# Optimization experiments

Measured on AMD Instinct MI355X. Metric: run time of the kernel, lower is better.

## Reference

```python
import jax, jax.numpy as jnp
import numpy as np

B, T = 64, 512
VOCAB, E, H = 20, 64, 128
D = 2 * H            # 256, bidirectional LSTM output dim
NH, KD = 8, D // 8   # 8 heads, key_dim 32
DU, OUT = 256, 128
NEG = -1e9


def _lstm_scan(x, mask, W, U, b):
    # x: [B,T,E], mask: [B,T] bool. Keras gate order: i, f, g(c), o.
    Bb = x.shape[0]
    Hh = U.shape[0]
    def step(carry, inp):
        h, c = carry
        xt, mt = inp                      # [B,E], [B]
        z = xt @ W + h @ U + b            # [B,4H]
        i, f, g, o = jnp.split(z, 4, axis=-1)
        c_new = jax.nn.sigmoid(f) * c + jax.nn.sigmoid(i) * jnp.tanh(g)
        h_new = jax.nn.sigmoid(o) * jnp.tanh(c_new)
        m = mt[:, None]
        h = jnp.where(m, h_new, h)        # freeze state/output on masked steps
        c = jnp.where(m, c_new, c)
        return (h, c), h
    h0 = jnp.zeros((Bb, Hh), x.dtype)
    _, ys = jax.lax.scan(step, (h0, h0), (jnp.swapaxes(x, 0, 1), mask.T))
    return jnp.swapaxes(ys, 0, 1)         # [B,T,H]


def setup_inputs() -> dict:
    key = jax.random.key(0)
    ks = jax.random.split(key, 24)
    g = lambda k, shape, s: (jax.random.normal(k, shape, jnp.float32) * s)
    inp = {
        'sequences': jax.random.randint(ks[0], (B, T), 0, VOCAB),
        'emb': g(ks[1], (VOCAB, E), 0.05),
        # forward LSTM
        'Wf': g(ks[2], (E, 4 * H), 0.05), 'Uf': g(ks[3], (H, 4 * H), 0.05), 'bf': jnp.zeros((4 * H,), jnp.float32),
        # backward LSTM
        'Wb': g(ks[4], (E, 4 * H), 0.05), 'Ub': g(ks[5], (H, 4 * H), 0.05), 'bb': jnp.zeros((4 * H,), jnp.float32),
        # MHA projections
        'Wq': g(ks[6], (D, NH, KD), 0.05), 'bq': jnp.zeros((NH, KD), jnp.float32),
        'Wk': g(ks[7], (D, NH, KD), 0.05), 'bk': jnp.zeros((NH, KD), jnp.float32),
        'Wv': g(ks[8], (D, NH, KD), 0.05), 'bv': jnp.zeros((NH, KD), jnp.float32),
        'Wo': g(ks[9], (NH, KD, D), 0.05), 'bo': jnp.zeros((D,), jnp.float32),
        # MLP head (input is concat of avg+max pool -> 2*D)
        'W1': g(ks[10], (2 * D, DU), 0.05), 'b1': jnp.zeros((DU,), jnp.float32),
        'W2': g(ks[11], (DU, DU // 2), 0.05), 'b2': jnp.zeros((DU // 2,), jnp.float32),
        'W3': g(ks[12], (DU // 2, OUT), 0.05), 'b3': jnp.zeros((OUT,), jnp.float32),
    }
    return inp


def _forward(sequences, emb, Wf, Uf, bf, Wb, Ub, bb, Wq, bq, Wk, bk, Wv, bv, Wo, bo, W1, b1, W2, b2, W3, b3):
    mask = sequences != 0                       # mask_zero=True
    x = emb[sequences]                          # [B,T,E]
    fwd = _lstm_scan(x, mask, Wf, Uf, bf)
    bwd = _lstm_scan(x[:, ::-1], mask[:, ::-1], Wb, Ub, bb)[:, ::-1]
    h = jnp.concatenate([fwd, bwd], axis=-1)    # [B,T,D]
    # Multi-head self-attention (key-masked, Keras MHA math)
    q = jnp.einsum('btd,dhk->bthk', h, Wq) + bq
    k = jnp.einsum('btd,dhk->bthk', h, Wk) + bk
    v = jnp.einsum('btd,dhk->bthk', h, Wv) + bv
    scores = jnp.einsum('bthk,bshk->bhts', q, k) / jnp.sqrt(jnp.float32(KD))
    scores = jnp.where(mask[:, None, None, :], scores, NEG)
    attn = jax.nn.softmax(scores, axis=-1)      # [B,H,T,T]
    ctx = jnp.einsum('bhts,bshk->bthk', attn, v)
    att = jnp.einsum('bthk,hkd->btd', ctx, Wo) + bo   # [B,T,D]
    # dual pooling (masked mean + masked max)
    mf = mask[..., None].astype(att.dtype)
    avg = (att * mf).sum(axis=1) / jnp.maximum(mf.sum(axis=1), 1.0)
    mx = jnp.where(mask[..., None], att, NEG).max(axis=1)
    p = jnp.concatenate([avg, mx], axis=-1)     # [B,2D]
    x1 = jax.nn.relu(p @ W1 + b1)
    x2 = jax.nn.relu(x1 @ W2 + b2)
    return x2 @ W3 + b3                         # [B,OUT]


def reference(sequences, emb, Wf, Uf, bf, Wb, Ub, bb, Wq, bq, Wk, bk, Wv, bv, Wo, bo, W1, b1, W2, b2, W3, b3):
    return _forward(sequences, emb, Wf, Uf, bf, Wb, Ub, bb, Wq, bq, Wk, bk, Wv, bv, Wo, bo, W1, b1, W2, b2, W3, b3)
```

## Files before the change

### kernel.cpp

```cpp
#include <hip/hip_runtime.h>
#include <math.h>

#define B_ 64
#define T_ 512
#define E_ 64
#define H_ 128
#define NH_ 8
#define KD_ 32
#define BT_ (B_ * T_)
#define NEG_ -1e9f

typedef __attribute__((ext_vector_type(8))) short bf16x8_t;
typedef __attribute__((ext_vector_type(4))) float f32x4_t;
typedef unsigned short ushort_t;
typedef unsigned int uint_t;

__device__ __forceinline__ float sigmoidf_(float x) {
    return 1.f / (1.f + __expf(-x));
}
__device__ __forceinline__ float tanhf_(float x) {
    return 1.f - 2.f / (1.f + __expf(2.f * x));
}

__device__ __forceinline__ ushort_t bf16_rne(float x) {
    uint_t u = __float_as_uint(x);
    uint_t r = (u + 0x7FFFu + ((u >> 16) & 1u)) >> 16;
    return (ushort_t)r;
}
__device__ __forceinline__ float bf16_to_f(ushort_t h) {
    return __uint_as_float(((uint_t)h) << 16);
}
__device__ __forceinline__ void split_bf16(float x, ushort_t& h, ushort_t& l) {
    h = bf16_rne(x);
    l = bf16_rne(x - bf16_to_f(h));
}

__device__ __forceinline__ float qswap1(float x) {
    return __int_as_float(__builtin_amdgcn_mov_dpp(__float_as_int(x), 0xB1, 0xF, 0xF, true));
}
__device__ __forceinline__ float qswap2(float x) {
    return __int_as_float(__builtin_amdgcn_mov_dpp(__float_as_int(x), 0x4E, 0xF, 0xF, true));
}

template <bool GATHER, bool PERM>
__global__ __launch_bounds__(256, 3) void gemm_f32(
    const float* __restrict__ A, const int* __restrict__ gidx,
    const float* __restrict__ emb, const float* __restrict__ Bm,
    const float* __restrict__ bias, float* __restrict__ C,
    int M, int N, int K)
{
    __shared__ __align__(16) float As[16][132];
    __shared__ __align__(16) float Bs[16][128];
    const int tid = threadIdx.x;
    const int tx = tid & 15, ty = tid >> 4;
    const int ntn = N >> 7;
    const int bm = blockIdx.x / ntn, bn = blockIdx.x % ntn;
    const int m0 = bm << 7, n0 = bn << 7;

    float acc[8][8];
#pragma unroll
    for (int i = 0; i < 8; ++i)
#pragma unroll
        for (int j = 0; j < 8; ++j) acc[i][j] = 0.f;

    const int ac4 = (tid & 3) << 2;
    const int ar  = tid >> 2;
    const int bc4 = (tid & 31) << 2;
    const int br  = tid >> 5;

    for (int k0 = 0; k0 < K; k0 += 16) {
        __syncthreads();
#pragma unroll
        for (int p = 0; p < 2; ++p) {
            const int r = ar + p * 64;
            const int gm = m0 + r;
            const float* src = GATHER
                ? (emb + (size_t)gidx[gm] * K + (k0 + ac4))
                : (A + (size_t)gm * K + (k0 + ac4));
            float4 v = *(const float4*)src;
            As[ac4 + 0][r] = v.x; As[ac4 + 1][r] = v.y;
            As[ac4 + 2][r] = v.z; As[ac4 + 3][r] = v.w;
        }
#pragma unroll
        for (int p = 0; p < 2; ++p) {
            const int rr = br + p * 8;
            if (PERM) {
                const float* brow = Bm + (size_t)(k0 + rr) * N;
                const int base = (n0 >> 2) + (tid & 31);
                Bs[rr][bc4 + 0] = brow[base];
                Bs[rr][bc4 + 1] = brow[128 + base];
                Bs[rr][bc4 + 2] = brow[256 + base];
                Bs[rr][bc4 + 3] = brow[384 + base];
            } else {
                float4 v = *(const float4*)(Bm + (size_t)(k0 + rr) * N + (n0 + bc4));
                *(float4*)&Bs[rr][bc4] = v;
            }
        }
        __syncthreads();
#pragma unroll
        for (int k = 0; k < 16; ++k) {
            float a[8], b[8];
            *(float4*)&a[0] = *(const float4*)&As[k][ty << 3];
            *(float4*)&a[4] = *(const float4*)&As[k][(ty << 3) + 4];
            *(float4*)&b[0] = *(const float4*)&Bs[k][tx << 3];
            *(float4*)&b[4] = *(const float4*)&Bs[k][(tx << 3) + 4];
#pragma unroll
            for (int i = 0; i < 8; ++i)
#pragma unroll
                for (int j = 0; j < 8; ++j)
                    acc[i][j] = fmaf(a[i], b[j], acc[i][j]);
        }
    }

    float bv[8];
#pragma unroll
    for (int j = 0; j < 8; ++j) {
        const int n = n0 + (tx << 3) + j;
        bv[j] = PERM ? bias[((n & 3) << 7) + (n >> 2)] : bias[n];
    }
#pragma unroll
    for (int i = 0; i < 8; ++i) {
        float* dst = C + (size_t)(m0 + (ty << 3) + i) * N + n0 + (tx << 3);
        float4 o0 = { acc[i][0] + bv[0], acc[i][1] + bv[1],
                      acc[i][2] + bv[2], acc[i][3] + bv[3] };
        float4 o1 = { acc[i][4] + bv[4], acc[i][5] + bv[5],
                      acc[i][6] + bv[6], acc[i][7] + bv[7] };
        *(float4*)dst = o0;
        *(float4*)(dst + 4) = o1;
    }
}

__global__ void wconv(const float* __restrict__ W,
                      ushort_t* __restrict__ Bh, ushort_t* __restrict__ Bl)
{
    const int k = blockIdx.x, n = threadIdx.x;
    float v = W[k * 256 + n];
    ushort_t h, l;
    split_bf16(v, h, l);
    Bh[n * 256 + k] = h;
    Bl[n * 256 + k] = l;
}

__global__ __launch_bounds__(256, 2) void gemm_mfma3(
    const ushort_t* __restrict__ Ah, const ushort_t* __restrict__ Al,
    const ushort_t* __restrict__ Bh, const ushort_t* __restrict__ Bl,
    const float* __restrict__ bias, float* __restrict__ C,
    int M, int N)
{
    __shared__ __align__(16) ushort_t Alds[2][128 * 40];
    __shared__ __align__(16) ushort_t Blds[2][128 * 40];

    const int tid = threadIdx.x;
    const int ntn = N >> 7;
    const int bm = blockIdx.x / ntn, bn = blockIdx.x % ntn;
    const int m0 = bm << 7, n0 = bn << 7;

    const int w = tid >> 6;
    const int wr = w >> 1, wc = w & 1;
    const int lane = tid & 63;
    const int fr = lane & 15, kg = lane >> 4;

    const int sr = tid >> 1;
    const int sh = (tid & 1) << 4;

    f32x4_t acc[4][4];
#pragma unroll
    for (int i = 0; i < 4; ++i)
#pragma unroll
        for (int j = 0; j < 4; ++j) acc[i][j] = (f32x4_t){0.f, 0.f, 0.f, 0.f};

    for (int ks = 0; ks < 8; ++ks) {
        const int k0 = ks << 5;
        __syncthreads();
        {
            const size_t ga = (size_t)(m0 + sr) * 256 + k0 + sh;
            const size_t gb = (size_t)(n0 + sr) * 256 + k0 + sh;
            const int ld = sr * 40 + sh;
            const uint4* pah = (const uint4*)(Ah + ga);
            const uint4* pal = (const uint4*)(Al + ga);
            const uint4* pbh = (const uint4*)(Bh + gb);
            const uint4* pbl = (const uint4*)(Bl + gb);
            uint4* qah = (uint4*)&Alds[0][ld];
            uint4* qal = (uint4*)&Alds[1][ld];
            uint4* qbh = (uint4*)&Blds[0][ld];
            uint4* qbl = (uint4*)&Blds[1][ld];
            qah[0] = pah[0]; qah[1] = pah[1];
            qal[0] = pal[0]; qal[1] = pal[1];
            qbh[0] = pbh[0]; qbh[1] = pbh[1];
            qbl[0] = pbl[0]; qbl[1] = pbl[1];
        }
        __syncthreads();

        bf16x8_t ah[4], al[4], bh[4], bl[4];
#pragma unroll
        for (int i = 0; i < 4; ++i) {
            const int ra = (wr * 64 + i * 16 + fr) * 40 + kg * 8;
            const int rb = (wc * 64 + i * 16 + fr) * 40 + kg * 8;
            ah[i] = *(const bf16x8_t*)&Alds[0][ra];
            al[i] = *(const bf16x8_t*)&Alds[1][ra];
            bh[i] = *(const bf16x8_t*)&Blds[0][rb];
            bl[i] = *(const bf16x8_t*)&Blds[1][rb];
        }
#pragma unroll
        for (int i = 0; i < 4; ++i)
#pragma unroll
            for (int j = 0; j < 4; ++j) {
                acc[i][j] = __builtin_amdgcn_mfma_f32_16x16x32_bf16(
                    ah[i], bh[j], acc[i][j], 0, 0, 0);
                acc[i][j] = __builtin_amdgcn_mfma_f32_16x16x32_bf16(
                    ah[i], bl[j], acc[i][j], 0, 0, 0);
                acc[i][j] = __builtin_amdgcn_mfma_f32_16x16x32_bf16(
                    al[i], bh[j], acc[i][j], 0, 0, 0);
            }
    }

#pragma unroll
    for (int j = 0; j < 4; ++j) {
        const int col = n0 + wc * 64 + j * 16 + fr;
        const float bv = bias[col];
#pragma unroll
        for (int i = 0; i < 4; ++i) {
#pragma unroll
            for (int r = 0; r < 4; ++r) {
                const int row = m0 + wr * 64 + i * 16 + kg * 4 + r;
                C[(size_t)row * N + col] = acc[i][j][r] + bv;
            }
        }
    }
}

__global__ __launch_bounds__(512, 1) void lstm_scan(
    const int* __restrict__ seq,
    const float* __restrict__ xwf, const float* __restrict__ xwb,
    const float* __restrict__ Uf, const float* __restrict__ Ub,
    ushort_t* __restrict__ hch, ushort_t* __restrict__ hcl)
{
    const int w = blockIdx.x;
    const int dir = w & 1, b = w >> 1;
    const float* xw = dir ? xwb : xwf;
    const float* U  = dir ? Ub  : Uf;
    const int tid = threadIdx.x;
    const int jj = tid >> 2, ks = tid & 3;

    __shared__ __align__(16) float hbuf[2][4][36];
    __shared__ float mkl[T_];

    float u[4][32];
#pragma unroll
    for (int g = 0; g < 4; ++g)
#pragma unroll
        for (int kk = 0; kk < 32; ++kk)
            u[g][kk] = U[(size_t)(32 * ks + kk) * 512 + g * 128 + jj];

    mkl[tid] = (seq[b * T_ + tid] != 0) ? 1.f : 0.f;
    if (tid < 2 * 4 * 36) ((float*)hbuf)[tid] = 0.f;

    float h_cur = 0.f, c_cur = 0.f;
    ushort_t* hoh = hch + (size_t)b * T_ * 256 + dir * 128;
    ushort_t* hol = hcl + (size_t)b * T_ * 256 + dir * 128;
    const float* xr = xw + (size_t)b * T_ * 512;

    __syncthreads();

    int te = dir ? (T_ - 1) : 0;
    float4 xwv = *(const float4*)&xr[(size_t)te * 512 + jj * 4];

    int p = 0;
    for (int t = 0; t < T_; ++t) {
        const int te_n  = dir ? (te - 1) : (te + 1);
        const int te_pf = (t == T_ - 1) ? te : te_n;
        const float4 xw_n = *(const float4*)&xr[(size_t)te_pf * 512 + jj * 4];

        float a0 = 0.f, a1 = 0.f, a2 = 0.f, a3 = 0.f;
        const float* hc = hbuf[p][ks];
#pragma unroll
        for (int c = 0; c < 8; ++c) {
            const float4 h4 = *(const float4*)&hc[c * 4];
            a0 = fmaf(h4.x, u[0][c*4+0], a0); a0 = fmaf(h4.y, u[0][c*4+1], a0);
            a0 = fmaf(h4.z, u[0][c*4+2], a0); a0 = fmaf(h4.w, u[0][c*4+3], a0);
            a1 = fmaf(h4.x, u[1][c*4+0], a1); a1 = fmaf(h4.y, u[1][c*4+1], a1);
            a1 = fmaf(h4.z, u[1][c*4+2], a1); a1 = fmaf(h4.w, u[1][c*4+3], a1);
            a2 = fmaf(h4.x, u[2][c*4+0], a2); a2 = fmaf(h4.y, u[2][c*4+1], a2);
            a2 = fmaf(h4.z, u[2][c*4+2], a2); a2 = fmaf(h4.w, u[2][c*4+3], a2);
            a3 = fmaf(h4.x, u[3][c*4+0], a3); a3 = fmaf(h4.y, u[3][c*4+1], a3);
            a3 = fmaf(h4.z, u[3][c*4+2], a3); a3 = fmaf(h4.w, u[3][c*4+3], a3);
        }
        a0 += qswap1(a0); a0 += qswap2(a0);
        a1 += qswap1(a1); a1 += qswap2(a1);
        a2 += qswap1(a2); a2 += qswap2(a2);
        a3 += qswap1(a3); a3 += qswap2(a3);

        const float zi = xwv.x + a0, zf = xwv.y + a1;
        const float zg = xwv.z + a2, zo = xwv.w + a3;
        const float cn = fmaf(sigmoidf_(zf), c_cur, sigmoidf_(zi) * tanhf_(zg));
        const float hn = sigmoidf_(zo) * tanhf_(cn);
        const float m  = mkl[te];
        const float hm = (m > 0.5f) ? hn : h_cur;
        c_cur = (m > 0.5f) ? cn : c_cur;
        h_cur = hm;

        if ((jj >> 5) == ks) hbuf[1 - p][ks][jj & 31] = hm;
        if (ks == 0) {
            ushort_t hh, hl;
            split_bf16(hm, hh, hl);
            hoh[(size_t)te * 256 + jj] = hh;
            hol[(size_t)te * 256 + jj] = hl;
        }
        __syncthreads();
        p ^= 1; te = te_n; xwv = xw_n;
    }
}

__global__ __launch_bounds__(256, 2) void attn_fused(
    const int* __restrict__ seq,
    const float* __restrict__ q, const float* __restrict__ kk,
    const float* __restrict__ vv,
    ushort_t* __restrict__ cxh, ushort_t* __restrict__ cxl)
{
    const int wg = blockIdx.x;
    const int b = wg >> 3, h = wg & 7;
    const int tid = threadIdx.x;

    __shared__ __align__(16) float Ks[16][32];
    __shared__ __align__(16) float Vs[16][32];
    __shared__ float mk[16];

    float qA[32], qB[32];
    {
        const float* qp  = q + (((size_t)(b * T_) + tid) * NH_ + h) * KD_;
        const float* qp2 = qp + (size_t)256 * NH_ * KD_;
#pragma unroll
        for (int k = 0; k < 32; k += 4) {
            float4 v0 = *(const float4*)(qp + k);
            float4 v1 = *(const float4*)(qp2 + k);
            qA[k] = v0.x; qA[k + 1] = v0.y; qA[k + 2] = v0.z; qA[k + 3] = v0.w;
            qB[k] = v1.x; qB[k + 1] = v1.y; qB[k + 2] = v1.z; qB[k + 3] = v1.w;
        }
    }
    float ctxA[32], ctxB[32];
#pragma unroll
    for (int k = 0; k < 32; ++k) { ctxA[k] = 0.f; ctxB[k] = 0.f; }
    float mA = -1e30f, mB = -1e30f, lA = 0.f, lB = 0.f;

    const int lr = (tid & 127) >> 3;
    const int lc = (tid & 7) << 2;
    const bool loadV = (tid >= 128);

    for (int c = 0; c < T_ / 16; ++c) {
        const int s0 = c << 4;
        __syncthreads();
        {
            const float* src = (loadV ? vv : kk) +
                (((size_t)(b * T_) + s0 + lr) * NH_ + h) * KD_ + lc;
            float4 v = *(const float4*)src;
            if (loadV) *(float4*)&Vs[lr][lc] = v;
            else       *(float4*)&Ks[lr][lc] = v;
            if (tid < 16) mk[tid] = (seq[b * T_ + s0 + tid] != 0) ? 0.f : 1.f;
        }
        __syncthreads();

        float sA[16], sB[16];
#pragma unroll
        for (int s = 0; s < 16; ++s) {
            float dA = 0.f, dB = 0.f;
#pragma unroll
            for (int k = 0; k < 32; k += 4) {
                float4 k4 = *(const float4*)&Ks[s][k];
                dA = fmaf(k4.x, qA[k], dA); dA = fmaf(k4.y, qA[k + 1], dA);
                dA = fmaf(k4.z, qA[k + 2], dA); dA = fmaf(k4.w, qA[k + 3], dA);
                dB = fmaf(k4.x, qB[k], dB); dB = fmaf(k4.y, qB[k + 1], dB);
                dB = fmaf(k4.z, qB[k + 2], dB); dB = fmaf(k4.w, qB[k + 3], dB);
            }
            const float SCL = 0.17677669529663687f;
            const bool masked = (mk[s] > 0.5f);
            sA[s] = masked ? NEG_ : dA * SCL;
            sB[s] = masked ? NEG_ : dB * SCL;
        }
        float cmA = sA[0], cmB = sB[0];
#pragma unroll
        for (int s = 1; s < 16; ++s) {
            cmA = fmaxf(cmA, sA[s]); cmB = fmaxf(cmB, sB[s]);
        }
        const float mnA = fmaxf(mA, cmA), mnB = fmaxf(mB, cmB);
        const float alA = __expf(mA - mnA), alB = __expf(mB - mnB);
        float psA = 0.f, psB = 0.f;
#pragma unroll
        for (int s = 0; s < 16; ++s) {
            float pa = __expf(sA[s] - mnA); sA[s] = pa; psA += pa;
            float pb = __expf(sB[s] - mnB); sB[s] = pb; psB += pb;
        }
        lA = fmaf(lA, alA, psA); lB = fmaf(lB, alB, psB);
        mA = mnA; mB = mnB;
#pragma unroll
        for (int k = 0; k < 32; ++k) { ctxA[k] *= alA; ctxB[k] *= alB; }
#pragma unroll
        for (int s = 0; s < 16; ++s) {
#pragma unroll
            for (int k = 0; k < 32; k += 4) {
                float4 v4 = *(const float4*)&Vs[s][k];
                ctxA[k]     = fmaf(sA[s], v4.x, ctxA[k]);
                ctxA[k + 1] = fmaf(sA[s], v4.y, ctxA[k + 1]);
                ctxA[k + 2] = fmaf(sA[s], v4.z, ctxA[k + 2]);
                ctxA[k + 3] = fmaf(sA[s], v4.w, ctxA[k + 3]);
                ctxB[k]     = fmaf(sB[s], v4.x, ctxB[k]);
                ctxB[k + 1] = fmaf(sB[s], v4.y, ctxB[k + 1]);
                ctxB[k + 2] = fmaf(sB[s], v4.z, ctxB[k + 2]);
                ctxB[k + 3] = fmaf(sB[s], v4.w, ctxB[k + 3]);
            }
        }
    }

    const float iA = 1.f / lA, iB = 1.f / lB;
    ushort_t* chA = cxh + (((size_t)(b * T_) + tid) * NH_ + h) * KD_;
    ushort_t* clA = cxl + (((size_t)(b * T_) + tid) * NH_ + h) * KD_;
    ushort_t* chB = chA + (size_t)256 * NH_ * KD_;
    ushort_t* clB = clA + (size_t)256 * NH_ * KD_;
#pragma unroll
    for (int k = 0; k < 32; ++k) {
        ushort_t hA, lA_, hB, lB_;
        split_bf16(ctxA[k] * iA, hA, lA_);
        split_bf16(ctxB[k] * iB, hB, lB_);
        chA[k] = hA; clA[k] = lA_;
        chB[k] = hB; clB[k] = lB_;
    }
}

__global__ void pool_kernel(const int* __restrict__ seq,
                            const float* __restrict__ att,
                            float* __restrict__ p)
{
    const int b = blockIdx.x;
    const int d = threadIdx.x;
    __shared__ float mk[T_];
    for (int t = d; t < T_; t += 256)
        mk[t] = (seq[b * T_ + t] != 0) ? 1.f : 0.f;
    __syncthreads();
    float sum = 0.f, mx = NEG_, cnt = 0.f;
    for (int t = 0; t < T_; ++t) {
        const float a = att[((size_t)b * T_ + t) * 256 + d];
        const float m = mk[t];
        cnt += m;
        sum = fmaf(m, a, sum);
        mx = fmaxf(mx, (m > 0.5f) ? a : NEG_);
    }
    p[b * 512 + d] = sum / fmaxf(cnt, 1.f);
    p[b * 512 + 256 + d] = mx;
}

__global__ void mlp_kernel(const float* __restrict__ p,
                           const float* __restrict__ W1, const float* __restrict__ b1,
                           const float* __restrict__ W2, const float* __restrict__ b2,
                           const float* __restrict__ W3, const float* __restrict__ b3,
                           float* __restrict__ out)
{
    const int b = blockIdx.x;
    const int tid = threadIdx.x;
    __shared__ float pl[512];
    __shared__ float x1l[256];
    __shared__ float x2l[128];
    pl[tid] = p[b * 512 + tid];
    pl[tid + 256] = p[b * 512 + 256 + tid];
    __syncthreads();
    {
        float acc = b1[tid];
        for (int k = 0; k < 512; ++k) acc = fmaf(pl[k], W1[k * 256 + tid], acc);
        x1l[tid] = fmaxf(acc, 0.f);
    }
    __syncthreads();
    if (tid < 128) {
        float acc = b2[tid];
        for (int k = 0; k < 256; ++k) acc = fmaf(x1l[k], W2[k * 128 + tid], acc);
        x2l[tid] = fmaxf(acc, 0.f);
    }
    __syncthreads();
    if (tid < 128) {
        float acc = b3[tid];
        for (int k = 0; k < 128; ++k) acc = fmaf(x2l[k], W3[k * 128 + tid], acc);
        out[b * 128 + tid] = acc;
    }
}

extern "C" void kernel_launch(void* const* d_in, const int* in_sizes, int n_in,
                              void* d_out, int out_size, void* d_ws, size_t ws_size,
                              hipStream_t stream)
{
    (void)in_sizes; (void)n_in; (void)out_size; (void)ws_size;
    const int*   seq = (const int*)d_in[0];
    const float* emb = (const float*)d_in[1];
    const float* Wf  = (const float*)d_in[2];
    const float* Uf  = (const float*)d_in[3];
    const float* bf  = (const float*)d_in[4];
    const float* Wb  = (const float*)d_in[5];
    const float* Ub  = (const float*)d_in[6];
    const float* bb  = (const float*)d_in[7];
    const float* Wq  = (const float*)d_in[8];
    const float* bq  = (const float*)d_in[9];
    const float* Wk  = (const float*)d_in[10];
    const float* bk  = (const float*)d_in[11];
    const float* Wv  = (const float*)d_in[12];
    const float* bv  = (const float*)d_in[13];
    const float* Wo  = (const float*)d_in[14];
    const float* bo  = (const float*)d_in[15];
    const float* W1  = (const float*)d_in[16];
    const float* b1  = (const float*)d_in[17];
    const float* W2  = (const float*)d_in[18];
    const float* b2  = (const float*)d_in[19];
    const float* W3  = (const float*)d_in[20];
    const float* b3  = (const float*)d_in[21];
    float* out = (float*)d_out;
    float* ws  = (float*)d_ws;

    float* xw_f = ws;
    float* xw_b = ws + 16777216;
    float* qb   = ws;
    float* kb   = ws + 8388608;
    float* vb   = ws + 16777216;
    ushort_t* cxh = (ushort_t*)(ws + 25165824);
    ushort_t* cxl = cxh + (size_t)BT_ * 256;
    ushort_t* hch = (ushort_t*)(ws + 33554432);
    ushort_t* hcl = hch + (size_t)BT_ * 256;
    float* attb = ws + 33554432;
    float* pb   = ws + 41943040;
    ushort_t* wt = (ushort_t*)(ws + 41975808);
    ushort_t* Wqh = wt + 0 * 65536, *Wql = wt + 1 * 65536;
    ushort_t* Wkh = wt + 2 * 65536, *Wkl = wt + 3 * 65536;
    ushort_t* Wvh = wt + 4 * 65536, *Wvl = wt + 5 * 65536;
    ushort_t* Woh = wt + 6 * 65536, *Wol = wt + 7 * 65536;

    const dim3 blk256(256), blk512(512);

    wconv<<<dim3(256), blk256, 0, stream>>>(Wq, Wqh, Wql);
    wconv<<<dim3(256), blk256, 0, stream>>>(Wk, Wkh, Wkl);
    wconv<<<dim3(256), blk256, 0, stream>>>(Wv, Wvh, Wvl);
    wconv<<<dim3(256), blk256, 0, stream>>>(Wo, Woh, Wol);

    gemm_f32<true, true><<<dim3((BT_ / 128) * (512 / 128)), blk256, 0, stream>>>(
        nullptr, seq, emb, Wf, bf, xw_f, BT_, 512, 64);
    gemm_f32<true, true><<<dim3((BT_ / 128) * (512 / 128)), blk256, 0, stream>>>(
        nullptr, seq, emb, Wb, bb, xw_b, BT_, 512, 64);

    lstm_scan<<<dim3(128), blk512, 0, stream>>>(seq, xw_f, xw_b, Uf, Ub, hch, hcl);

    gemm_mfma3<<<dim3((BT_ / 128) * 2), blk256, 0, stream>>>(
        hch, hcl, Wqh, Wql, bq, qb, BT_, 256);
    gemm_mfma3<<<dim3((BT_ / 128) * 2), blk256, 0, stream>>>(
        hch, hcl, Wkh, Wkl, bk, kb, BT_, 256);
    gemm_mfma3<<<dim3((BT_ / 128) * 2), blk256, 0, stream>>>(
        hch, hcl, Wvh, Wvl, bv, vb, BT_, 256);

    attn_fused<<<dim3(B_ * NH_), blk256, 0, stream>>>(seq, qb, kb, vb, cxh, cxl);

    gemm_mfma3<<<dim3((BT_ / 128) * 2), blk256, 0, stream>>>(
        cxh, cxl, Woh, Wol, bo, attb, BT_, 256);

    pool_kernel<<<dim3(B_), blk256, 0, stream>>>(seq, attb, pb);
    mlp_kernel<<<dim3(B_), blk256, 0, stream>>>(pb, W1, b1, W2, b2, W3, b3, out);
}
```

Measured before the change: 911.4 us.

## Precompute vocab-by-gate input table and fuse prep, pool and MLP kernels

Since the vocabulary has only 20 tokens, the input projection emb@W+b is computed once per token into a 20x512 table per direction, replacing two large gather GEMMs over all B*T positions. The LSTM scan then reads the table by token id and derives the mask from the token directly. The recurrent matvec is rewritten with packed two-wide float FMAs, and the four weight-conversion launches are merged with the table build into one prep kernel. Pooling and the MLP are fused into a single kernel, which removes the pooled intermediate buffer and a launch.

```diff
diff --git a/kernel.cpp b/kernel.cpp
--- a/kernel.cpp
+++ b/kernel.cpp
@@ -12,6 +12,7 @@
 
 typedef __attribute__((ext_vector_type(8))) short bf16x8_t;
 typedef __attribute__((ext_vector_type(4))) float f32x4_t;
+typedef __attribute__((ext_vector_type(2))) float f32x2_t;
 typedef unsigned short ushort_t;
 typedef unsigned int uint_t;
 
@@ -42,103 +43,44 @@
     return __int_as_float(__builtin_amdgcn_mov_dpp(__float_as_int(x), 0x4E, 0xF, 0xF, true));
 }
 
-template <bool GATHER, bool PERM>
-__global__ __launch_bounds__(256, 3) void gemm_f32(
-    const float* __restrict__ A, const int* __restrict__ gidx,
-    const float* __restrict__ emb, const float* __restrict__ Bm,
-    const float* __restrict__ bias, float* __restrict__ C,
-    int M, int N, int K)
-{
-    __shared__ __align__(16) float As[16][132];
-    __shared__ __align__(16) float Bs[16][128];
-    const int tid = threadIdx.x;
-    const int tx = tid & 15, ty = tid >> 4;
-    const int ntn = N >> 7;
-    const int bm = blockIdx.x / ntn, bn = blockIdx.x % ntn;
-    const int m0 = bm << 7, n0 = bn << 7;
-
-    float acc[8][8];
-#pragma unroll
-    for (int i = 0; i < 8; ++i)
-#pragma unroll
-        for (int j = 0; j < 8; ++j) acc[i][j] = 0.f;
-
-    const int ac4 = (tid & 3) << 2;
-    const int ar  = tid >> 2;
-    const int bc4 = (tid & 31) << 2;
-    const int br  = tid >> 5;
-
-    for (int k0 = 0; k0 < K; k0 += 16) {
-        __syncthreads();
-#pragma unroll
-        for (int p = 0; p < 2; ++p) {
-            const int r = ar + p * 64;
-            const int gm = m0 + r;
-            const float* src = GATHER
-                ? (emb + (size_t)gidx[gm] * K + (k0 + ac4))
-                : (A + (size_t)gm * K + (k0 + ac4));
-            float4 v = *(const float4*)src;
-            As[ac4 + 0][r] = v.x; As[ac4 + 1][r] = v.y;
-            As[ac4 + 2][r] = v.z; As[ac4 + 3][r] = v.w;
-        }
-#pragma unroll
-        for (int p = 0; p < 2; ++p) {
-            const int rr = br + p * 8;
-            if (PERM) {
-                const float* brow = Bm + (size_t)(k0 + rr) * N;
-                const int base = (n0 >> 2) + (tid & 31);
-                Bs[rr][bc4 + 0] = brow[base];
-                Bs[rr][bc4 + 1] = brow[128 + base];
-                Bs[rr][bc4 + 2] = brow[256 + base];
-                Bs[rr][bc4 + 3] = brow[384 + base];
-            } else {
-                float4 v = *(const float4*)(Bm + (size_t)(k0 + rr) * N + (n0 + bc4));
-                *(float4*)&Bs[rr][bc4] = v;
-            }
-        }
-        __syncthreads();
-#pragma unroll
-        for (int k = 0; k < 16; ++k) {
-            float a[8], b[8];
-            *(float4*)&a[0] = *(const float4*)&As[k][ty << 3];
-            *(float4*)&a[4] = *(const float4*)&As[k][(ty << 3) + 4];
-            *(float4*)&b[0] = *(const float4*)&Bs[k][tx << 3];
-            *(float4*)&b[4] = *(const float4*)&Bs[k][(tx << 3) + 4];
-#pragma unroll
-            for (int i = 0; i < 8; ++i)
-#pragma unroll
-                for (int j = 0; j < 8; ++j)
-                    acc[i][j] = fmaf(a[i], b[j], acc[i][j]);
-        }
-    }
-
-    float bv[8];
-#pragma unroll
-    for (int j = 0; j < 8; ++j) {
-        const int n = n0 + (tx << 3) + j;
-        bv[j] = PERM ? bias[((n & 3) << 7) + (n >> 2)] : bias[n];
-    }
-#pragma unroll
-    for (int i = 0; i < 8; ++i) {
-        float* dst = C + (size_t)(m0 + (ty << 3) + i) * N + n0 + (tx << 3);
-        float4 o0 = { acc[i][0] + bv[0], acc[i][1] + bv[1],
-                      acc[i][2] + bv[2], acc[i][3] + bv[3] };
-        float4 o1 = { acc[i][4] + bv[4], acc[i][5] + bv[5],
-                      acc[i][6] + bv[6], acc[i][7] + bv[7] };
-        *(float4*)dst = o0;
-        *(float4*)(dst + 4) = o1;
-    }
-}
-
-__global__ void wconv(const float* __restrict__ W,
-                      ushort_t* __restrict__ Bh, ushort_t* __restrict__ Bl)
-{
-    const int k = blockIdx.x, n = threadIdx.x;
-    float v = W[k * 256 + n];
-    ushort_t h, l;
-    split_bf16(v, h, l);
-    Bh[n * 256 + k] = h;
-    Bl[n * 256 + k] = l;
+__global__ void prep_kernel(
+    const float* __restrict__ emb,
+    const float* __restrict__ Wf, const float* __restrict__ bf,
+    const float* __restrict__ Wb, const float* __restrict__ bb,
+    const float* __restrict__ Wq, const float* __restrict__ Wk,
+    const float* __restrict__ Wv, const float* __restrict__ Wo,
+    ushort_t* __restrict__ Wqh, ushort_t* __restrict__ Wql,
+    ushort_t* __restrict__ Wkh, ushort_t* __restrict__ Wkl,
+    ushort_t* __restrict__ Wvh, ushort_t* __restrict__ Wvl,
+    ushort_t* __restrict__ Woh, ushort_t* __restrict__ Wol,
+    float* __restrict__ embWf, float* __restrict__ embWb)
+{
+    const int blk = blockIdx.x, tid = threadIdx.x;
+    if (blk < 1024) {
+        const int m = blk >> 8, k = blk & 255;
+        const float* W = (m == 0) ? Wq : (m == 1) ? Wk : (m == 2) ? Wv : Wo;
+        ushort_t* Bh = (m == 0) ? Wqh : (m == 1) ? Wkh : (m == 2) ? Wvh : Woh;
+        ushort_t* Bl = (m == 0) ? Wql : (m == 1) ? Wkl : (m == 2) ? Wvl : Wol;
+        float v = W[k * 256 + tid];
+        ushort_t h, l;
+        split_bf16(v, h, l);
+        Bh[tid * 256 + k] = h;
+        Bl[tid * 256 + k] = l;
+    } else {
+        const int e = blk - 1024;
+        const int dir = e >> 1, half = e & 1;
+        const float* W = dir ? Wb : Wf;
+        const float* bias = dir ? bb : bf;
+        float* dst = dir ? embWb : embWf;
+        const int np = half * 256 + tid;
+        const int gin = ((np & 3) << 7) + (np >> 2);
+        for (int v = 0; v < 20; ++v) {
+            float acc = bias[gin];
+            for (int k = 0; k < 64; ++k)
+                acc = fmaf(emb[v * 64 + k], W[k * 512 + gin], acc);
+            dst[v * 512 + np] = acc;
+        }
+    }
 }
 
 __global__ __launch_bounds__(256, 2) void gemm_mfma3(
@@ -231,60 +173,64 @@
 
 __global__ __launch_bounds__(512, 1) void lstm_scan(
     const int* __restrict__ seq,
-    const float* __restrict__ xwf, const float* __restrict__ xwb,
+    const float* __restrict__ embWf, const float* __restrict__ embWb,
     const float* __restrict__ Uf, const float* __restrict__ Ub,
     ushort_t* __restrict__ hch, ushort_t* __restrict__ hcl)
 {
     const int w = blockIdx.x;
     const int dir = w & 1, b = w >> 1;
-    const float* xw = dir ? xwb : xwf;
+    const float* eW = dir ? embWb : embWf;
     const float* U  = dir ? Ub  : Uf;
     const int tid = threadIdx.x;
     const int jj = tid >> 2, ks = tid & 3;
 
     __shared__ __align__(16) float hbuf[2][4][36];
-    __shared__ float mkl[T_];
-
-    float u[4][32];
+    __shared__ int tkl[T_];
+
+    f32x2_t u2[4][16];
 #pragma unroll
     for (int g = 0; g < 4; ++g)
 #pragma unroll
-        for (int kk = 0; kk < 32; ++kk)
-            u[g][kk] = U[(size_t)(32 * ks + kk) * 512 + g * 128 + jj];
-
-    mkl[tid] = (seq[b * T_ + tid] != 0) ? 1.f : 0.f;
+        for (int kk = 0; kk < 16; ++kk) {
+            const int kb_ = 32 * ks + 2 * kk;
+            u2[g][kk] = (f32x2_t){
+                U[(size_t)kb_ * 512 + g * 128 + jj],
+                U[(size_t)(kb_ + 1) * 512 + g * 128 + jj] };
+        }
+
+    tkl[tid] = seq[b * T_ + tid];
     if (tid < 2 * 4 * 36) ((float*)hbuf)[tid] = 0.f;
 
     float h_cur = 0.f, c_cur = 0.f;
     ushort_t* hoh = hch + (size_t)b * T_ * 256 + dir * 128;
     ushort_t* hol = hcl + (size_t)b * T_ * 256 + dir * 128;
-    const float* xr = xw + (size_t)b * T_ * 512;
 
     __syncthreads();
 
     int te = dir ? (T_ - 1) : 0;
-    float4 xwv = *(const float4*)&xr[(size_t)te * 512 + jj * 4];
+    int tok = tkl[te];
+    float4 xwv = *(const float4*)&eW[tok * 512 + jj * 4];
 
     int p = 0;
     for (int t = 0; t < T_; ++t) {
         const int te_n  = dir ? (te - 1) : (te + 1);
         const int te_pf = (t == T_ - 1) ? te : te_n;
-        const float4 xw_n = *(const float4*)&xr[(size_t)te_pf * 512 + jj * 4];
-
-        float a0 = 0.f, a1 = 0.f, a2 = 0.f, a3 = 0.f;
-        const float* hc = hbuf[p][ks];
-#pragma unroll
-        for (int c = 0; c < 8; ++c) {
-            const float4 h4 = *(const float4*)&hc[c * 4];
-            a0 = fmaf(h4.x, u[0][c*4+0], a0); a0 = fmaf(h4.y, u[0][c*4+1], a0);
-            a0 = fmaf(h4.z, u[0][c*4+2], a0); a0 = fmaf(h4.w, u[0][c*4+3], a0);
-            a1 = fmaf(h4.x, u[1][c*4+0], a1); a1 = fmaf(h4.y, u[1][c*4+1], a1);
-            a1 = fmaf(h4.z, u[1][c*4+2], a1); a1 = fmaf(h4.w, u[1][c*4+3], a1);
-            a2 = fmaf(h4.x, u[2][c*4+0], a2); a2 = fmaf(h4.y, u[2][c*4+1], a2);
-            a2 = fmaf(h4.z, u[2][c*4+2], a2); a2 = fmaf(h4.w, u[2][c*4+3], a2);
-            a3 = fmaf(h4.x, u[3][c*4+0], a3); a3 = fmaf(h4.y, u[3][c*4+1], a3);
-            a3 = fmaf(h4.z, u[3][c*4+2], a3); a3 = fmaf(h4.w, u[3][c*4+3], a3);
-        }
+        const int tok_n = tkl[te_pf];
+        const float4 xw_n = *(const float4*)&eW[tok_n * 512 + jj * 4];
+
+        f32x2_t ac0 = {0.f, 0.f}, ac1 = {0.f, 0.f};
+        f32x2_t ac2 = {0.f, 0.f}, ac3 = {0.f, 0.f};
+        const f32x2_t* hc2 = (const f32x2_t*)hbuf[p][ks];
+#pragma unroll
+        for (int c = 0; c < 16; ++c) {
+            const f32x2_t h2 = hc2[c];
+            ac0 = __builtin_elementwise_fma(h2, u2[0][c], ac0);
+            ac1 = __builtin_elementwise_fma(h2, u2[1][c], ac1);
+            ac2 = __builtin_elementwise_fma(h2, u2[2][c], ac2);
+            ac3 = __builtin_elementwise_fma(h2, u2[3][c], ac3);
+        }
+        float a0 = ac0.x + ac0.y, a1 = ac1.x + ac1.y;
+        float a2 = ac2.x + ac2.y, a3 = ac3.x + ac3.y;
         a0 += qswap1(a0); a0 += qswap2(a0);
         a1 += qswap1(a1); a1 += qswap2(a1);
         a2 += qswap1(a2); a2 += qswap2(a2);
@@ -294,9 +240,9 @@
         const float zg = xwv.z + a2, zo = xwv.w + a3;
         const float cn = fmaf(sigmoidf_(zf), c_cur, sigmoidf_(zi) * tanhf_(zg));
         const float hn = sigmoidf_(zo) * tanhf_(cn);
-        const float m  = mkl[te];
-        const float hm = (m > 0.5f) ? hn : h_cur;
-        c_cur = (m > 0.5f) ? cn : c_cur;
+        const bool mt = (tok != 0);
+        const float hm = mt ? hn : h_cur;
+        c_cur = mt ? cn : c_cur;
         h_cur = hm;
 
         if ((jj >> 5) == ks) hbuf[1 - p][ks][jj & 31] = hm;
@@ -307,7 +253,7 @@
             hol[(size_t)te * 256 + jj] = hl;
         }
         __syncthreads();
-        p ^= 1; te = te_n; xwv = xw_n;
+        p ^= 1; te = te_n; tok = tok_n; xwv = xw_n;
     }
 }
 
@@ -425,42 +371,36 @@
     }
 }
 
-__global__ void pool_kernel(const int* __restrict__ seq,
-                            const float* __restrict__ att,
-                            float* __restrict__ p)
+__global__ __launch_bounds__(256) void poolmlp_kernel(
+    const int* __restrict__ seq, const float* __restrict__ att,
+    const float* __restrict__ W1, const float* __restrict__ b1,
+    const float* __restrict__ W2, const float* __restrict__ b2,
+    const float* __restrict__ W3, const float* __restrict__ b3,
+    float* __restrict__ out)
 {
     const int b = blockIdx.x;
-    const int d = threadIdx.x;
+    const int tid = threadIdx.x;
     __shared__ float mk[T_];
-    for (int t = d; t < T_; t += 256)
+    __shared__ float pl[512];
+    __shared__ float x1l[256];
+    __shared__ float x2l[128];
+
+    for (int t = tid; t < T_; t += 256)
         mk[t] = (seq[b * T_ + t] != 0) ? 1.f : 0.f;
     __syncthreads();
+
     float sum = 0.f, mx = NEG_, cnt = 0.f;
     for (int t = 0; t < T_; ++t) {
-        const float a = att[((size_t)b * T_ + t) * 256 + d];
+        const float a = att[((size_t)b * T_ + t) * 256 + tid];
         const float m = mk[t];
         cnt += m;
         sum = fmaf(m, a, sum);
         mx = fmaxf(mx, (m > 0.5f) ? a : NEG_);
     }
-    p[b * 512 + d] = sum / fmaxf(cnt, 1.f);
-    p[b * 512 + 256 + d] = mx;
-}
-
-__global__ void mlp_kernel(const float* __restrict__ p,
-                           const float* __restrict__ W1, const float* __restrict__ b1,
-                           const float* __restrict__ W2, const float* __restrict__ b2,
-                           const float* __restrict__ W3, const float* __restrict__ b3,
-                           float* __restrict__ out)
-{
-    const int b = blockIdx.x;
-    const int tid = threadIdx.x;
-    __shared__ float pl[512];
-    __shared__ float x1l[256];
-    __shared__ float x2l[128];
-    pl[tid] = p[b * 512 + tid];
-    pl[tid + 256] = p[b * 512 + 256 + tid];
+    pl[tid] = sum / fmaxf(cnt, 1.f);
+    pl[256 + tid] = mx;
     __syncthreads();
+
     {
         float acc = b1[tid];
         for (int k = 0; k < 512; ++k) acc = fmaf(pl[k], W1[k * 256 + tid], acc);
@@ -510,8 +450,6 @@
     float* out = (float*)d_out;
     float* ws  = (float*)d_ws;
 
-    float* xw_f = ws;
-    float* xw_b = ws + 16777216;
     float* qb   = ws;
     float* kb   = ws + 8388608;
     float* vb   = ws + 16777216;
@@ -520,26 +458,22 @@
     ushort_t* hch = (ushort_t*)(ws + 33554432);
     ushort_t* hcl = hch + (size_t)BT_ * 256;
     float* attb = ws + 33554432;
-    float* pb   = ws + 41943040;
-    ushort_t* wt = (ushort_t*)(ws + 41975808);
+    ushort_t* wt = (ushort_t*)(ws + 41943040);
     ushort_t* Wqh = wt + 0 * 65536, *Wql = wt + 1 * 65536;
     ushort_t* Wkh = wt + 2 * 65536, *Wkl = wt + 3 * 65536;
     ushort_t* Wvh = wt + 4 * 65536, *Wvl = wt + 5 * 65536;
     ushort_t* Woh = wt + 6 * 65536, *Wol = wt + 7 * 65536;
+    float* embWf = ws + 41943040 + 262144;
+    float* embWb = embWf + 20 * 512;
 
     const dim3 blk256(256), blk512(512);
 
-    wconv<<<dim3(256), blk256, 0, stream>>>(Wq, Wqh, Wql);
-    wconv<<<dim3(256), blk256, 0, stream>>>(Wk, Wkh, Wkl);
-    wconv<<<dim3(256), blk256, 0, stream>>>(Wv, Wvh, Wvl);
-    wconv<<<dim3(256), blk256, 0, stream>>>(Wo, Woh, Wol);
-
-    gemm_f32<true, true><<<dim3((BT_ / 128) * (512 / 128)), blk256, 0, stream>>>(
-        nullptr, seq, emb, Wf, bf, xw_f, BT_, 512, 64);
-    gemm_f32<true, true><<<dim3((BT_ / 128) * (512 / 128)), blk256, 0, stream>>>(
-        nullptr, seq, emb, Wb, bb, xw_b, BT_, 512, 64);
-
-    lstm_scan<<<dim3(128), blk512, 0, stream>>>(seq, xw_f, xw_b, Uf, Ub, hch, hcl);
+    prep_kernel<<<dim3(1028), blk256, 0, stream>>>(
+        emb, Wf, bf, Wb, bb, Wq, Wk, Wv, Wo,
+        Wqh, Wql, Wkh, Wkl, Wvh, Wvl, Woh, Wol, embWf, embWb);
+
+    lstm_scan<<<dim3(128), blk512, 0, stream>>>(
+        seq, embWf, embWb, Uf, Ub, hch, hcl);
 
     gemm_mfma3<<<dim3((BT_ / 128) * 2), blk256, 0, stream>>>(
         hch, hcl, Wqh, Wql, bq, qb, BT_, 256);
@@ -553,6 +487,6 @@
     gemm_mfma3<<<dim3((BT_ / 128) * 2), blk256, 0, stream>>>(
         cxh, cxl, Woh, Wol, bo, attb, BT_, 256);
 
-    pool_kernel<<<dim3(B_), blk256, 0, stream>>>(seq, attb, pb);
-    mlp_kernel<<<dim3(B_), blk256, 0, stream>>>(pb, W1, b1, W2, b2, W3, b3, out);
-}
+    poolmlp_kernel<<<dim3(B_), blk256, 0, stream>>>(
+        seq, attb, W1, b1, W2, b2, W3, b3, out);
+}
```

Measured after the change: 945.2 us. 3.7% more time.
